# Optimization experiments

Hardware: AMD Instinct MI355X
Metric: run time of the kernel (lower is better)

The kernel has to match this reference:

```python
import jax, jax.numpy as jnp
import numpy as np

N_MELS, HIDDEN, HEAD_DIM = 80, 128, 64


def _gru_step(h, gx_t, w_hh, b_hh):
    # PyTorch GRU cell math. gx_t = x_t @ W_ih^T + b_ih, precomputed. [B, 3H]
    H = h.shape[-1]
    gh = h @ w_hh.T + b_hh  # [B, 3H]
    r = jax.nn.sigmoid(gx_t[:, :H] + gh[:, :H])
    z = jax.nn.sigmoid(gx_t[:, H:2 * H] + gh[:, H:2 * H])
    n = jnp.tanh(gx_t[:, 2 * H:] + r * gh[:, 2 * H:])
    return (1.0 - z) * n + z * h


def setup_inputs() -> dict:
    key = jax.random.key(0)
    ks = jax.random.split(key, 14)
    s = 1.0 / np.sqrt(HIDDEN)
    u = lambda k, shape, sc: jax.random.uniform(k, shape, jnp.float32, -sc, sc)
    return {
        "x": jax.random.normal(ks[0], (128, 1500, N_MELS), dtype=jnp.float32),
        # forward-direction GRU params
        "w_ih_f": u(ks[1], (3 * HIDDEN, N_MELS), s),
        "w_hh_f": u(ks[2], (3 * HIDDEN, HIDDEN), s),
        "b_ih_f": u(ks[3], (3 * HIDDEN,), s),
        "b_hh_f": u(ks[4], (3 * HIDDEN,), s),
        # backward-direction GRU params
        "w_ih_b": u(ks[5], (3 * HIDDEN, N_MELS), s),
        "w_hh_b": u(ks[6], (3 * HIDDEN, HIDDEN), s),
        "b_ih_b": u(ks[7], (3 * HIDDEN,), s),
        "b_hh_b": u(ks[8], (3 * HIDDEN,), s),
        # MLP head: Linear(2H, 64) -> ReLU -> Linear(64, 1)
        "w1": u(ks[9], (HEAD_DIM, 2 * HIDDEN), 1.0 / np.sqrt(2 * HIDDEN)),
        "b1": u(ks[10], (HEAD_DIM,), 1.0 / np.sqrt(2 * HIDDEN)),
        "w2": u(ks[11], (1, HEAD_DIM), 1.0 / np.sqrt(HEAD_DIM)),
        "b2": u(ks[12], (1,), 1.0 / np.sqrt(HEAD_DIM)),
    }


def reference(x, w_ih_f, w_hh_f, b_ih_f, b_hh_f, w_ih_b, w_hh_b, b_ih_b, b_hh_b, w1, b1, w2, b2):
    B, T, _ = x.shape
    h0 = jnp.zeros((B, HIDDEN), dtype=x.dtype)

    # Forward direction: last output = final hidden state after full scan.
    # Precompute input projections for all timesteps in one GEMM.
    gx_f = jnp.einsum('bti,gi->tbg', x, w_ih_f) + b_ih_f  # [T, B, 3H]
    h_f, _ = jax.lax.scan(lambda h, g: (_gru_step(h, g, w_hh_f, b_hh_f), None), h0, gx_f)

    # Backward direction: out[:, -1, H:] in PyTorch is the backward hidden
    # after processing ONLY x[:, -1] (the reverse scan's first step), so a
    # single GRU step from h0 reproduces it exactly.
    gx_b_last = x[:, -1, :] @ w_ih_b.T + b_ih_b  # [B, 3H]
    h_b = _gru_step(h0, gx_b_last, w_hh_b, b_hh_b)

    last = jnp.concatenate([h_f, h_b], axis=-1)  # [B, 2H]
    # Head (eval mode: dropout is identity)
    hdn = jax.nn.relu(last @ w1.T + b1)
    out = hdn @ w2.T + b2  # [B, 1]
    return out[:, 0]
```

## Files before the change

kernel.cpp:

```cpp
#include <hip/hip_runtime.h>

#define B 128
#define T 1500
#define NI 80
#define H 128
#define G 384
#define GT 64
#define NTT 128

typedef float v2f __attribute__((ext_vector_type(2)));

__device__ __forceinline__ float sigf(float x) { return 1.0f / (1.0f + __expf(-x)); }
__device__ __forceinline__ float tanhfast(float x) { return 1.0f - 2.0f / (1.0f + __expf(2.0f * x)); }
__device__ __forceinline__ v2f pkfma(v2f a, v2f b, v2f c) { return __builtin_elementwise_fma(a, b, c); }

__device__ __forceinline__ float sum8(float v) {
    int a = __builtin_bit_cast(int, v);
    float m = __builtin_bit_cast(float, __builtin_amdgcn_update_dpp(0, a, 0x141, 0xF, 0xF, true));
    float s = v + m;
    a = __builtin_bit_cast(int, s);
    m = __builtin_bit_cast(float, __builtin_amdgcn_update_dpp(0, a, 0x1B, 0xF, 0xF, true));
    s = s + m;
    a = __builtin_bit_cast(int, s);
    m = __builtin_bit_cast(float, __builtin_amdgcn_update_dpp(0, a, 0xB1, 0xF, 0xF, true));
    return s + m;
}

__global__ __launch_bounds__(256, 2)
void gx_gemm_kernel(const float* __restrict__ x, const float* __restrict__ w_ih,
                    const float* __restrict__ b_ih, float* __restrict__ gxT,
                    int t0, int ct) {
    __shared__ __align__(16) float wT[80][GT + 2];
    __shared__ __align__(16) float xT[80][NTT + 4];
    __shared__ float bias_s[GT];
    int tid = threadIdx.x;
    int b = blockIdx.z;
    int g0b = blockIdx.y * GT;
    int tt0 = blockIdx.x * NTT;

    for (int i = tid; i < GT * 20; i += 256) {
        int g = i & (GT - 1);
        int kc = i >> 6;
        float4 v = *(const float4*)(w_ih + (size_t)(g0b + g) * NI + 4 * kc);
        wT[4 * kc + 0][g] = v.x; wT[4 * kc + 1][g] = v.y;
        wT[4 * kc + 2][g] = v.z; wT[4 * kc + 3][g] = v.w;
    }
    for (int i = tid; i < NTT * 20; i += 256) {
        int c = i & (NTT - 1);
        int kc = i >> 7;
        int tt = tt0 + c; if (tt > ct - 1) tt = ct - 1;
        float4 v = *(const float4*)(x + ((size_t)b * T + (size_t)(t0 + tt)) * NI + 4 * kc);
        xT[4 * kc + 0][c] = v.x; xT[4 * kc + 1][c] = v.y;
        xT[4 * kc + 2][c] = v.z; xT[4 * kc + 3][c] = v.w;
    }
    if (tid < GT) bias_s[tid] = b_ih[g0b + tid];
    __syncthreads();

    int gi = tid & 15;
    int ti = tid >> 4;
    v2f acc[4][4];
#pragma unroll
    for (int r = 0; r < 4; ++r)
#pragma unroll
        for (int j = 0; j < 4; ++j) acc[r][j] = v2f{0.f, 0.f};

#pragma unroll 2
    for (int k = 0; k < 80; ++k) {
        const v2f* wv = (const v2f*)&wT[k][4 * gi];
        v2f w01 = wv[0], w23 = wv[1];
        const float4* xv = (const float4*)&xT[k][8 * ti];
        float4 x03 = xv[0], x47 = xv[1];
        v2f xp0 = {x03.x, x03.y}, xp1 = {x03.z, x03.w};
        v2f xp2 = {x47.x, x47.y}, xp3 = {x47.z, x47.w};
        float wr[4] = {w01.x, w01.y, w23.x, w23.y};
#pragma unroll
        for (int r = 0; r < 4; ++r) {
            v2f ws = {wr[r], wr[r]};
            acc[r][0] = pkfma(ws, xp0, acc[r][0]);
            acc[r][1] = pkfma(ws, xp1, acc[r][1]);
            acc[r][2] = pkfma(ws, xp2, acc[r][2]);
            acc[r][3] = pkfma(ws, xp3, acc[r][3]);
        }
    }
    __syncthreads();

    float (*ot)[NTT + 4] = (float (*)[NTT + 4])xT;
#pragma unroll
    for (int r = 0; r < 4; ++r) {
        float bias = bias_s[4 * gi + r];
#pragma unroll
        for (int j = 0; j < 4; ++j) {
            float2 o; o.x = acc[r][j].x + bias; o.y = acc[r][j].y + bias;
            *(float2*)&ot[4 * gi + r][8 * ti + 2 * j] = o;
        }
    }
    __syncthreads();

    for (int i = tid; i < GT * (NTT / 4); i += 256) {
        int row = i >> 5;
        int col = i & 31;
        int t = tt0 + 4 * col;
        if (t < ct) {
            float4 v = *(const float4*)&ot[row][4 * col];
            *(float4*)(gxT + ((size_t)b * G + g0b + row) * ct + t) = v;
        }
    }
}

__global__ __launch_bounds__(512)
__attribute__((amdgpu_waves_per_eu(2, 2)))
void scan_kernel(const float* __restrict__ gxT, const float* __restrict__ w_hh,
                 const float* __restrict__ b_hh, float* __restrict__ h_state,
                 int ct, int first, int last,
                 const float* __restrict__ x,
                 const float* __restrict__ w_ih_b, const float* __restrict__ b_ih_b,
                 const float* __restrict__ b_hh_b,
                 const float* __restrict__ w1, const float* __restrict__ b1,
                 const float* __restrict__ w2, const float* __restrict__ b2,
                 float* __restrict__ out) {
    int b = blockIdx.x;
    int tid = threadIdx.x;
    int jp = tid >> 3;
    int q = tid & 7;
    int j0 = jp, j1 = jp + 64;
    int jsel = (q < 4) ? j0 : j1;
    int hsel = ((jsel >> 4) * 20) + (jsel & 15);
    bool writer = (q & 3) == 0;

    __shared__ __align__(16) float hs[2][160];
    __shared__ __align__(16) float tail_gx[G];
    __shared__ __align__(16) float last_s[2 * H];
    __shared__ __align__(16) float xb_s[NI];

    v2f W0r[8], W0z[8], W0n[8], W1r[8], W1z[8], W1n[8];
    {
        const float* wb = w_hh + 16 * q;
        const v2f* p0 = (const v2f*)(wb + (size_t)j0 * H);
        const v2f* p1 = (const v2f*)(wb + (size_t)(j0 + H) * H);
        const v2f* p2 = (const v2f*)(wb + (size_t)(j0 + 2 * H) * H);
        const v2f* p3 = (const v2f*)(wb + (size_t)j1 * H);
        const v2f* p4 = (const v2f*)(wb + (size_t)(j1 + H) * H);
        const v2f* p5 = (const v2f*)(wb + (size_t)(j1 + 2 * H) * H);
#pragma unroll
        for (int i = 0; i < 8; ++i) {
            W0r[i] = p0[i]; W0z[i] = p1[i]; W0n[i] = p2[i];
            W1r[i] = p3[i]; W1z[i] = p4[i]; W1n[i] = p5[i];
        }
    }
#pragma unroll
    for (int i = 0; i < 8; ++i) {
        asm volatile("" : "+v"(W0r[i]), "+v"(W0z[i]), "+v"(W0n[i]),
                          "+v"(W1r[i]), "+v"(W1z[i]), "+v"(W1n[i]));
    }
    float br = b_hh[jsel], bz = b_hh[jsel + H], bn = b_hh[jsel + 2 * H];

    float h_cur = 0.f;
    if (!first) h_cur = h_state[b * H + jsel];
    if (writer) hs[0][hsel] = h_cur;

    const float* gp0 = gxT + ((size_t)b * G + jsel) * ct;
    const float* gp1 = gp0 + (size_t)H * ct;
    const float* gp2 = gp0 + (size_t)(2 * H) * ct;

    float4 A0, A1, A2, B0, B1, B2;
    A0 = *(const float4*)(gp0); A1 = *(const float4*)(gp1); A2 = *(const float4*)(gp2);
    {
        int t4 = (ct - 4 < 4) ? (ct - 4) : 4;
        B0 = *(const float4*)(gp0 + t4); B1 = *(const float4*)(gp1 + t4); B2 = *(const float4*)(gp2 + t4);
    }
    __syncthreads();

    auto dostep = [&](float g0, float g1, float g2, const float* SRC, float* DST) {
        const float4* hv4 = (const float4*)(SRC + 20 * q);
        float4 h0 = hv4[0], h1 = hv4[1], h2 = hv4[2], h3 = hv4[3];
        v2f a0r = {0.f, 0.f}, a0z = {0.f, 0.f}, a0n = {0.f, 0.f};
        v2f a1r = {0.f, 0.f}, a1z = {0.f, 0.f}, a1n = {0.f, 0.f};
        float4 hh[4] = {h0, h1, h2, h3};
#pragma unroll
        for (int i = 0; i < 4; ++i) {
            v2f hl = {hh[i].x, hh[i].y}, hg = {hh[i].z, hh[i].w};
            a0r = pkfma(W0r[2 * i], hl, a0r); a0r = pkfma(W0r[2 * i + 1], hg, a0r);
            a0z = pkfma(W0z[2 * i], hl, a0z); a0z = pkfma(W0z[2 * i + 1], hg, a0z);
            a0n = pkfma(W0n[2 * i], hl, a0n); a0n = pkfma(W0n[2 * i + 1], hg, a0n);
            a1r = pkfma(W1r[2 * i], hl, a1r); a1r = pkfma(W1r[2 * i + 1], hg, a1r);
            a1z = pkfma(W1z[2 * i], hl, a1z); a1z = pkfma(W1z[2 * i + 1], hg, a1z);
            a1n = pkfma(W1n[2 * i], hl, a1n); a1n = pkfma(W1n[2 * i + 1], hg, a1n);
        }
        float s0r = sum8(a0r.x + a0r.y), s0z = sum8(a0z.x + a0z.y), s0n = sum8(a0n.x + a0n.y);
        float s1r = sum8(a1r.x + a1r.y), s1z = sum8(a1z.x + a1z.y), s1n = sum8(a1n.x + a1n.y);
        bool lo = q < 4;
        float ar = lo ? s0r : s1r;
        float az = lo ? s0z : s1z;
        float an = lo ? s0n : s1n;
        float r = sigf(g0 + br + ar);
        float z = sigf(g1 + bz + az);
        float n = tanhfast(g2 + r * (bn + an));
        h_cur = n + z * (h_cur - n);
        if (writer) DST[hsel] = h_cur;
        asm volatile("s_waitcnt lgkmcnt(0)\n\ts_barrier" ::: "memory");
    };

    auto superstep = [&](int TL, float4& S0, float4& S1, float4& S2) {
        float l00 = S0.x, l01 = S0.y, l02 = S0.z, l03 = S0.w;
        float l10 = S1.x, l11 = S1.y, l12 = S1.z, l13 = S1.w;
        float l20 = S2.x, l21 = S2.y, l22 = S2.z, l23 = S2.w;
        int tpf = TL + 8; if (tpf > ct - 4) tpf = ct - 4;
        S0 = *(const float4*)(gp0 + tpf);
        S1 = *(const float4*)(gp1 + tpf);
        S2 = *(const float4*)(gp2 + tpf);
        dostep(l00, l10, l20, hs[0], hs[1]);
        dostep(l01, l11, l21, hs[1], hs[0]);
        dostep(l02, l12, l22, hs[0], hs[1]);
        dostep(l03, l13, l23, hs[1], hs[0]);
    };

    int tl = 0;
    for (; tl + 8 <= ct; tl += 8) {
        superstep(tl, A0, A1, A2);
        superstep(tl + 4, B0, B1, B2);
    }
    if (tl < ct) superstep(tl, A0, A1, A2);

    if (!last) {
        if (writer) h_state[b * H + jsel] = h_cur;
        return;
    }

    if (tid < NI) xb_s[tid] = x[((size_t)b * T + (T - 1)) * NI + tid];
    if (writer) last_s[jsel] = h_cur;
    __syncthreads();

    if (tid < G) {
        const float4* wbr = (const float4*)(w_ih_b + (size_t)tid * NI);
        const float4* xv = (const float4*)xb_s;
        float a0 = 0.f, a1 = 0.f, a2 = 0.f, a3 = 0.f;
#pragma unroll
        for (int i = 0; i < 20; ++i) {
            float4 wv = wbr[i]; float4 x4 = xv[i];
            a0 = fmaf(wv.x, x4.x, a0); a1 = fmaf(wv.y, x4.y, a1);
            a2 = fmaf(wv.z, x4.z, a2); a3 = fmaf(wv.w, x4.w, a3);
        }
        tail_gx[tid] = b_ih_b[tid] + ((a0 + a1) + (a2 + a3));
    }
    __syncthreads();

    if (tid < H) {
        float r = sigf(tail_gx[tid] + b_hh_b[tid]);
        float z = sigf(tail_gx[tid + H] + b_hh_b[tid + H]);
        float n = tanhfast(tail_gx[tid + 2 * H] + r * b_hh_b[tid + 2 * H]);
        last_s[H + tid] = (1.f - z) * n;
    }
    __syncthreads();

    if (tid < 64) {
        const float4* w1r = (const float4*)(w1 + (size_t)tid * 2 * H);
        const float4* lv = (const float4*)last_s;
        float a0 = 0.f, a1 = 0.f, a2 = 0.f, a3 = 0.f;
#pragma unroll
        for (int i = 0; i < 64; ++i) {
            float4 wv = w1r[i]; float4 l4 = lv[i];
            a0 = fmaf(wv.x, l4.x, a0); a1 = fmaf(wv.y, l4.y, a1);
            a2 = fmaf(wv.z, l4.z, a2); a3 = fmaf(wv.w, l4.w, a3);
        }
        float v = b1[tid] + ((a0 + a1) + (a2 + a3));
        v = fmaxf(v, 0.f) * w2[tid];
#pragma unroll
        for (int off = 32; off > 0; off >>= 1) v += __shfl_down(v, off);
        if (tid == 0) out[b] = v + b2[0];
    }
}

extern "C" void kernel_launch(void* const* d_in, const int* in_sizes, int n_in,
                              void* d_out, int out_size, void* d_ws, size_t ws_size,
                              hipStream_t stream) {
    (void)in_sizes; (void)n_in; (void)out_size;
    const float* x      = (const float*)d_in[0];
    const float* w_ih_f = (const float*)d_in[1];
    const float* w_hh_f = (const float*)d_in[2];
    const float* b_ih_f = (const float*)d_in[3];
    const float* b_hh_f = (const float*)d_in[4];
    const float* w_ih_b = (const float*)d_in[5];
    const float* w_hh_b = (const float*)d_in[6];
    const float* b_ih_b = (const float*)d_in[7];
    const float* b_hh_b = (const float*)d_in[8];
    const float* w1     = (const float*)d_in[9];
    const float* b1     = (const float*)d_in[10];
    const float* w2     = (const float*)d_in[11];
    const float* b2     = (const float*)d_in[12];
    (void)w_hh_b;
    float* out = (float*)d_out;

    float* h_state = (float*)d_ws;
    float* gxbuf = h_state + B * H;
    size_t hbytes = (size_t)B * H * sizeof(float);
    size_t avail = ws_size > hbytes ? ws_size - hbytes : 0;
    long long chunkT = (long long)(avail / ((size_t)B * G * sizeof(float)));
    chunkT &= ~3LL;
    if (chunkT > T) chunkT = T;
    if (chunkT < 4) chunkT = 4;

    for (int t0 = 0; t0 < T; t0 += (int)chunkT) {
        int ct = (T - t0 < (int)chunkT) ? (T - t0) : (int)chunkT;
        int ttiles = (ct + NTT - 1) / NTT;
        gx_gemm_kernel<<<dim3(ttiles, G / GT, B), dim3(256), 0, stream>>>(
            x, w_ih_f, b_ih_f, gxbuf, t0, ct);
        scan_kernel<<<dim3(B), dim3(512), 0, stream>>>(
            gxbuf, w_hh_f, b_hh_f, h_state, ct,
            (t0 == 0) ? 1 : 0, (t0 + ct >= T) ? 1 : 0,
            x, w_ih_b, b_ih_b, b_hh_b, w1, b1, w2, b2, out);
    }
}
```

Before: 1.118 ms.

## Fuse input-projection GEMM with recurrent scan and double-buffer chunks to overlap them

After: 962.8 us. 13.9% less time.

```diff
diff --git a/kernel.cpp b/kernel.cpp
--- a/kernel.cpp
+++ b/kernel.cpp
@@ -7,6 +7,10 @@
 #define G 384
 #define GT 64
 #define NTT 128
+
+#define WSZ (80 * (GT + 2))
+#define XSZ (80 * (NTT + 4))
+#define SMEM_FLOATS (WSZ + XSZ + GT)
 
 typedef float v2f __attribute__((ext_vector_type(2)));
 
@@ -26,247 +30,261 @@
     return s + m;
 }
 
-__global__ __launch_bounds__(256, 2)
-void gx_gemm_kernel(const float* __restrict__ x, const float* __restrict__ w_ih,
-                    const float* __restrict__ b_ih, float* __restrict__ gxT,
-                    int t0, int ct) {
-    __shared__ __align__(16) float wT[80][GT + 2];
-    __shared__ __align__(16) float xT[80][NTT + 4];
-    __shared__ float bias_s[GT];
-    int tid = threadIdx.x;
-    int b = blockIdx.z;
-    int g0b = blockIdx.y * GT;
-    int tt0 = blockIdx.x * NTT;
-
-    for (int i = tid; i < GT * 20; i += 256) {
-        int g = i & (GT - 1);
-        int kc = i >> 6;
-        float4 v = *(const float4*)(w_ih + (size_t)(g0b + g) * NI + 4 * kc);
-        wT[4 * kc + 0][g] = v.x; wT[4 * kc + 1][g] = v.y;
-        wT[4 * kc + 2][g] = v.z; wT[4 * kc + 3][g] = v.w;
-    }
-    for (int i = tid; i < NTT * 20; i += 256) {
-        int c = i & (NTT - 1);
-        int kc = i >> 7;
-        int tt = tt0 + c; if (tt > ct - 1) tt = ct - 1;
-        float4 v = *(const float4*)(x + ((size_t)b * T + (size_t)(t0 + tt)) * NI + 4 * kc);
-        xT[4 * kc + 0][c] = v.x; xT[4 * kc + 1][c] = v.y;
-        xT[4 * kc + 2][c] = v.z; xT[4 * kc + 3][c] = v.w;
-    }
-    if (tid < GT) bias_s[tid] = b_ih[g0b + tid];
-    __syncthreads();
-
-    int gi = tid & 15;
-    int ti = tid >> 4;
-    v2f acc[4][4];
-#pragma unroll
-    for (int r = 0; r < 4; ++r)
-#pragma unroll
-        for (int j = 0; j < 4; ++j) acc[r][j] = v2f{0.f, 0.f};
-
-#pragma unroll 2
-    for (int k = 0; k < 80; ++k) {
-        const v2f* wv = (const v2f*)&wT[k][4 * gi];
-        v2f w01 = wv[0], w23 = wv[1];
-        const float4* xv = (const float4*)&xT[k][8 * ti];
-        float4 x03 = xv[0], x47 = xv[1];
-        v2f xp0 = {x03.x, x03.y}, xp1 = {x03.z, x03.w};
-        v2f xp2 = {x47.x, x47.y}, xp3 = {x47.z, x47.w};
-        float wr[4] = {w01.x, w01.y, w23.x, w23.y};
-#pragma unroll
-        for (int r = 0; r < 4; ++r) {
-            v2f ws = {wr[r], wr[r]};
-            acc[r][0] = pkfma(ws, xp0, acc[r][0]);
-            acc[r][1] = pkfma(ws, xp1, acc[r][1]);
-            acc[r][2] = pkfma(ws, xp2, acc[r][2]);
-            acc[r][3] = pkfma(ws, xp3, acc[r][3]);
-        }
-    }
-    __syncthreads();
-
-    float (*ot)[NTT + 4] = (float (*)[NTT + 4])xT;
-#pragma unroll
-    for (int r = 0; r < 4; ++r) {
-        float bias = bias_s[4 * gi + r];
-#pragma unroll
-        for (int j = 0; j < 4; ++j) {
-            float2 o; o.x = acc[r][j].x + bias; o.y = acc[r][j].y + bias;
-            *(float2*)&ot[4 * gi + r][8 * ti + 2 * j] = o;
-        }
-    }
-    __syncthreads();
-
-    for (int i = tid; i < GT * (NTT / 4); i += 256) {
-        int row = i >> 5;
-        int col = i & 31;
-        int t = tt0 + 4 * col;
-        if (t < ct) {
-            float4 v = *(const float4*)&ot[row][4 * col];
-            *(float4*)(gxT + ((size_t)b * G + g0b + row) * ct + t) = v;
-        }
-    }
-}
-
 __global__ __launch_bounds__(512)
 __attribute__((amdgpu_waves_per_eu(2, 2)))
-void scan_kernel(const float* __restrict__ gxT, const float* __restrict__ w_hh,
-                 const float* __restrict__ b_hh, float* __restrict__ h_state,
-                 int ct, int first, int last,
-                 const float* __restrict__ x,
-                 const float* __restrict__ w_ih_b, const float* __restrict__ b_ih_b,
-                 const float* __restrict__ b_hh_b,
-                 const float* __restrict__ w1, const float* __restrict__ b1,
-                 const float* __restrict__ w2, const float* __restrict__ b2,
-                 float* __restrict__ out) {
-    int b = blockIdx.x;
+void fused_kernel(const float* __restrict__ x,
+                  const float* __restrict__ w_ih, const float* __restrict__ b_ih,
+                  const float* __restrict__ gx_read, int ct_read, int first, int last,
+                  float* __restrict__ gx_write, int t0_write, int ct_write,
+                  const float* __restrict__ w_hh, const float* __restrict__ b_hh,
+                  float* __restrict__ h_state,
+                  const float* __restrict__ w_ih_b, const float* __restrict__ b_ih_b,
+                  const float* __restrict__ b_hh_b,
+                  const float* __restrict__ w1, const float* __restrict__ b1,
+                  const float* __restrict__ w2, const float* __restrict__ b2,
+                  float* __restrict__ out) {
+    __shared__ __align__(16) float smem[SMEM_FLOATS];
     int tid = threadIdx.x;
-    int jp = tid >> 3;
-    int q = tid & 7;
-    int j0 = jp, j1 = jp + 64;
-    int jsel = (q < 4) ? j0 : j1;
-    int hsel = ((jsel >> 4) * 20) + (jsel & 15);
-    bool writer = (q & 3) == 0;
-
-    __shared__ __align__(16) float hs[2][160];
-    __shared__ __align__(16) float tail_gx[G];
-    __shared__ __align__(16) float last_s[2 * H];
-    __shared__ __align__(16) float xb_s[NI];
-
-    v2f W0r[8], W0z[8], W0n[8], W1r[8], W1z[8], W1n[8];
-    {
-        const float* wb = w_hh + 16 * q;
-        const v2f* p0 = (const v2f*)(wb + (size_t)j0 * H);
-        const v2f* p1 = (const v2f*)(wb + (size_t)(j0 + H) * H);
-        const v2f* p2 = (const v2f*)(wb + (size_t)(j0 + 2 * H) * H);
-        const v2f* p3 = (const v2f*)(wb + (size_t)j1 * H);
-        const v2f* p4 = (const v2f*)(wb + (size_t)(j1 + H) * H);
-        const v2f* p5 = (const v2f*)(wb + (size_t)(j1 + 2 * H) * H);
+    int scanBlocks = (ct_read > 0) ? B : 0;
+
+    if ((int)blockIdx.x < scanBlocks) {
+        const float* gxT = gx_read;
+        int ct = ct_read;
+        int b = blockIdx.x;
+        int jp = tid >> 3;
+        int q = tid & 7;
+        int j0 = jp, j1 = jp + 64;
+        int jsel = (q < 4) ? j0 : j1;
+        int hsel = ((jsel >> 4) * 20) + (jsel & 15);
+        bool writer = (q & 3) == 0;
+
+        float* hsA     = smem;
+        float* hsB     = smem + 160;
+        float* tail_gx = smem + 320;
+        float* last_s  = smem + 704;
+        float* xb_s    = smem + 960;
+
+        v2f W0r[8], W0z[8], W0n[8], W1r[8], W1z[8], W1n[8];
+        {
+            const float* wb = w_hh + 16 * q;
+            const v2f* p0 = (const v2f*)(wb + (size_t)j0 * H);
+            const v2f* p1 = (const v2f*)(wb + (size_t)(j0 + H) * H);
+            const v2f* p2 = (const v2f*)(wb + (size_t)(j0 + 2 * H) * H);
+            const v2f* p3 = (const v2f*)(wb + (size_t)j1 * H);
+            const v2f* p4 = (const v2f*)(wb + (size_t)(j1 + H) * H);
+            const v2f* p5 = (const v2f*)(wb + (size_t)(j1 + 2 * H) * H);
+#pragma unroll
+            for (int i = 0; i < 8; ++i) {
+                W0r[i] = p0[i]; W0z[i] = p1[i]; W0n[i] = p2[i];
+                W1r[i] = p3[i]; W1z[i] = p4[i]; W1n[i] = p5[i];
+            }
+        }
 #pragma unroll
         for (int i = 0; i < 8; ++i) {
-            W0r[i] = p0[i]; W0z[i] = p1[i]; W0n[i] = p2[i];
-            W1r[i] = p3[i]; W1z[i] = p4[i]; W1n[i] = p5[i];
-        }
-    }
-#pragma unroll
-    for (int i = 0; i < 8; ++i) {
-        asm volatile("" : "+v"(W0r[i]), "+v"(W0z[i]), "+v"(W0n[i]),
-                          "+v"(W1r[i]), "+v"(W1z[i]), "+v"(W1n[i]));
-    }
-    float br = b_hh[jsel], bz = b_hh[jsel + H], bn = b_hh[jsel + 2 * H];
-
-    float h_cur = 0.f;
-    if (!first) h_cur = h_state[b * H + jsel];
-    if (writer) hs[0][hsel] = h_cur;
-
-    const float* gp0 = gxT + ((size_t)b * G + jsel) * ct;
-    const float* gp1 = gp0 + (size_t)H * ct;
-    const float* gp2 = gp0 + (size_t)(2 * H) * ct;
-
-    float4 A0, A1, A2, B0, B1, B2;
-    A0 = *(const float4*)(gp0); A1 = *(const float4*)(gp1); A2 = *(const float4*)(gp2);
-    {
-        int t4 = (ct - 4 < 4) ? (ct - 4) : 4;
-        B0 = *(const float4*)(gp0 + t4); B1 = *(const float4*)(gp1 + t4); B2 = *(const float4*)(gp2 + t4);
-    }
-    __syncthreads();
-
-    auto dostep = [&](float g0, float g1, float g2, const float* SRC, float* DST) {
-        const float4* hv4 = (const float4*)(SRC + 20 * q);
-        float4 h0 = hv4[0], h1 = hv4[1], h2 = hv4[2], h3 = hv4[3];
-        v2f a0r = {0.f, 0.f}, a0z = {0.f, 0.f}, a0n = {0.f, 0.f};
-        v2f a1r = {0.f, 0.f}, a1z = {0.f, 0.f}, a1n = {0.f, 0.f};
-        float4 hh[4] = {h0, h1, h2, h3};
-#pragma unroll
-        for (int i = 0; i < 4; ++i) {
-            v2f hl = {hh[i].x, hh[i].y}, hg = {hh[i].z, hh[i].w};
-            a0r = pkfma(W0r[2 * i], hl, a0r); a0r = pkfma(W0r[2 * i + 1], hg, a0r);
-            a0z = pkfma(W0z[2 * i], hl, a0z); a0z = pkfma(W0z[2 * i + 1], hg, a0z);
-            a0n = pkfma(W0n[2 * i], hl, a0n); a0n = pkfma(W0n[2 * i + 1], hg, a0n);
-            a1r = pkfma(W1r[2 * i], hl, a1r); a1r = pkfma(W1r[2 * i + 1], hg, a1r);
-            a1z = pkfma(W1z[2 * i], hl, a1z); a1z = pkfma(W1z[2 * i + 1], hg, a1z);
-            a1n = pkfma(W1n[2 * i], hl, a1n); a1n = pkfma(W1n[2 * i + 1], hg, a1n);
-        }
-        float s0r = sum8(a0r.x + a0r.y), s0z = sum8(a0z.x + a0z.y), s0n = sum8(a0n.x + a0n.y);
-        float s1r = sum8(a1r.x + a1r.y), s1z = sum8(a1z.x + a1z.y), s1n = sum8(a1n.x + a1n.y);
-        bool lo = q < 4;
-        float ar = lo ? s0r : s1r;
-        float az = lo ? s0z : s1z;
-        float an = lo ? s0n : s1n;
-        float r = sigf(g0 + br + ar);
-        float z = sigf(g1 + bz + az);
-        float n = tanhfast(g2 + r * (bn + an));
-        h_cur = n + z * (h_cur - n);
-        if (writer) DST[hsel] = h_cur;
-        asm volatile("s_waitcnt lgkmcnt(0)\n\ts_barrier" ::: "memory");
-    };
-
-    auto superstep = [&](int TL, float4& S0, float4& S1, float4& S2) {
-        float l00 = S0.x, l01 = S0.y, l02 = S0.z, l03 = S0.w;
-        float l10 = S1.x, l11 = S1.y, l12 = S1.z, l13 = S1.w;
-        float l20 = S2.x, l21 = S2.y, l22 = S2.z, l23 = S2.w;
-        int tpf = TL + 8; if (tpf > ct - 4) tpf = ct - 4;
-        S0 = *(const float4*)(gp0 + tpf);
-        S1 = *(const float4*)(gp1 + tpf);
-        S2 = *(const float4*)(gp2 + tpf);
-        dostep(l00, l10, l20, hs[0], hs[1]);
-        dostep(l01, l11, l21, hs[1], hs[0]);
-        dostep(l02, l12, l22, hs[0], hs[1]);
-        dostep(l03, l13, l23, hs[1], hs[0]);
-    };
-
-    int tl = 0;
-    for (; tl + 8 <= ct; tl += 8) {
-        superstep(tl, A0, A1, A2);
-        superstep(tl + 4, B0, B1, B2);
-    }
-    if (tl < ct) superstep(tl, A0, A1, A2);
-
-    if (!last) {
-        if (writer) h_state[b * H + jsel] = h_cur;
+            asm volatile("" : "+v"(W0r[i]), "+v"(W0z[i]), "+v"(W0n[i]),
+                              "+v"(W1r[i]), "+v"(W1z[i]), "+v"(W1n[i]));
+        }
+        float br = b_hh[jsel], bz = b_hh[jsel + H], bn = b_hh[jsel + 2 * H];
+
+        float h_cur = 0.f;
+        if (!first) h_cur = h_state[b * H + jsel];
+        if (writer) hsA[hsel] = h_cur;
+
+        const float* gp0 = gxT + ((size_t)b * G + jsel) * ct;
+        const float* gp1 = gp0 + (size_t)H * ct;
+        const float* gp2 = gp0 + (size_t)(2 * H) * ct;
+
+        float4 A0, A1, A2, B0, B1, B2;
+        A0 = *(const float4*)(gp0); A1 = *(const float4*)(gp1); A2 = *(const float4*)(gp2);
+        {
+            int t4 = (ct - 4 < 4) ? (ct - 4) : 4;
+            B0 = *(const float4*)(gp0 + t4); B1 = *(const float4*)(gp1 + t4); B2 = *(const float4*)(gp2 + t4);
+        }
+        __syncthreads();
+
+        auto dostep = [&](float g0, float g1, float g2, const float* SRC, float* DST) {
+            const float4* hv4 = (const float4*)(SRC + 20 * q);
+            float4 h0 = hv4[0], h1 = hv4[1], h2 = hv4[2], h3 = hv4[3];
+            v2f a0r = {0.f, 0.f}, a0z = {0.f, 0.f}, a0n = {0.f, 0.f};
+            v2f a1r = {0.f, 0.f}, a1z = {0.f, 0.f}, a1n = {0.f, 0.f};
+            float4 hh[4] = {h0, h1, h2, h3};
+#pragma unroll
+            for (int i = 0; i < 4; ++i) {
+                v2f hl = {hh[i].x, hh[i].y}, hg = {hh[i].z, hh[i].w};
+                a0r = pkfma(W0r[2 * i], hl, a0r); a0r = pkfma(W0r[2 * i + 1], hg, a0r);
+                a0z = pkfma(W0z[2 * i], hl, a0z); a0z = pkfma(W0z[2 * i + 1], hg, a0z);
+                a0n = pkfma(W0n[2 * i], hl, a0n); a0n = pkfma(W0n[2 * i + 1], hg, a0n);
+                a1r = pkfma(W1r[2 * i], hl, a1r); a1r = pkfma(W1r[2 * i + 1], hg, a1r);
+                a1z = pkfma(W1z[2 * i], hl, a1z); a1z = pkfma(W1z[2 * i + 1], hg, a1z);
+                a1n = pkfma(W1n[2 * i], hl, a1n); a1n = pkfma(W1n[2 * i + 1], hg, a1n);
+            }
+            float s0r = sum8(a0r.x + a0r.y), s0z = sum8(a0z.x + a0z.y), s0n = sum8(a0n.x + a0n.y);
+            float s1r = sum8(a1r.x + a1r.y), s1z = sum8(a1z.x + a1z.y), s1n = sum8(a1n.x + a1n.y);
+            bool lo = q < 4;
+            float ar = lo ? s0r : s1r;
+            float az = lo ? s0z : s1z;
+            float an = lo ? s0n : s1n;
+            float r = sigf(g0 + br + ar);
+            float z = sigf(g1 + bz + az);
+            float n = tanhfast(g2 + r * (bn + an));
+            h_cur = n + z * (h_cur - n);
+            if (writer) DST[hsel] = h_cur;
+            asm volatile("s_waitcnt lgkmcnt(0)\n\ts_barrier" ::: "memory");
+        };
+
+        auto superstep = [&](int TL, float4& S0, float4& S1, float4& S2) {
+            float l00 = S0.x, l01 = S0.y, l02 = S0.z, l03 = S0.w;
+            float l10 = S1.x, l11 = S1.y, l12 = S1.z, l13 = S1.w;
+            float l20 = S2.x, l21 = S2.y, l22 = S2.z, l23 = S2.w;
+            int tpf = TL + 8; if (tpf > ct - 4) tpf = ct - 4;
+            S0 = *(const float4*)(gp0 + tpf);
+            S1 = *(const float4*)(gp1 + tpf);
+            S2 = *(const float4*)(gp2 + tpf);
+            dostep(l00, l10, l20, hsA, hsB);
+            dostep(l01, l11, l21, hsB, hsA);
+            dostep(l02, l12, l22, hsA, hsB);
+            dostep(l03, l13, l23, hsB, hsA);
+        };
+
+        int tl = 0;
+        for (; tl + 8 <= ct; tl += 8) {
+            superstep(tl, A0, A1, A2);
+            superstep(tl + 4, B0, B1, B2);
+        }
+        if (tl < ct) superstep(tl, A0, A1, A2);
+
+        if (!last) {
+            if (writer) h_state[b * H + jsel] = h_cur;
+            return;
+        }
+
+        if (tid < NI) xb_s[tid] = x[((size_t)b * T + (T - 1)) * NI + tid];
+        if (writer) last_s[jsel] = h_cur;
+        __syncthreads();
+
+        if (tid < G) {
+            const float4* wbr = (const float4*)(w_ih_b + (size_t)tid * NI);
+            const float4* xv = (const float4*)xb_s;
+            float a0 = 0.f, a1 = 0.f, a2 = 0.f, a3 = 0.f;
+#pragma unroll
+            for (int i = 0; i < 20; ++i) {
+                float4 wv = wbr[i]; float4 x4 = xv[i];
+                a0 = fmaf(wv.x, x4.x, a0); a1 = fmaf(wv.y, x4.y, a1);
+                a2 = fmaf(wv.z, x4.z, a2); a3 = fmaf(wv.w, x4.w, a3);
+            }
+            tail_gx[tid] = b_ih_b[tid] + ((a0 + a1) + (a2 + a3));
+        }
+        __syncthreads();
+
+        if (tid < H) {
+            float r = sigf(tail_gx[tid] + b_hh_b[tid]);
+            float z = sigf(tail_gx[tid + H] + b_hh_b[tid + H]);
+            float n = tanhfast(tail_gx[tid + 2 * H] + r * b_hh_b[tid + 2 * H]);
+            last_s[H + tid] = (1.f - z) * n;
+        }
+        __syncthreads();
+
+        if (tid < 64) {
+            const float4* w1r = (const float4*)(w1 + (size_t)tid * 2 * H);
+            const float4* lv = (const float4*)last_s;
+            float a0 = 0.f, a1 = 0.f, a2 = 0.f, a3 = 0.f;
+#pragma unroll
+            for (int i = 0; i < 64; ++i) {
+                float4 wv = w1r[i]; float4 l4 = lv[i];
+                a0 = fmaf(wv.x, l4.x, a0); a1 = fmaf(wv.y, l4.y, a1);
+                a2 = fmaf(wv.z, l4.z, a2); a3 = fmaf(wv.w, l4.w, a3);
+            }
+            float v = b1[tid] + ((a0 + a1) + (a2 + a3));
+            v = fmaxf(v, 0.f) * w2[tid];
+#pragma unroll
+            for (int off = 32; off > 0; off >>= 1) v += __shfl_down(v, off);
+            if (tid == 0) out[b] = v + b2[0];
+        }
         return;
     }
 
-    if (tid < NI) xb_s[tid] = x[((size_t)b * T + (T - 1)) * NI + tid];
-    if (writer) last_s[jsel] = h_cur;
-    __syncthreads();
-
-    if (tid < G) {
-        const float4* wbr = (const float4*)(w_ih_b + (size_t)tid * NI);
-        const float4* xv = (const float4*)xb_s;
-        float a0 = 0.f, a1 = 0.f, a2 = 0.f, a3 = 0.f;
-#pragma unroll
-        for (int i = 0; i < 20; ++i) {
-            float4 wv = wbr[i]; float4 x4 = xv[i];
-            a0 = fmaf(wv.x, x4.x, a0); a1 = fmaf(wv.y, x4.y, a1);
-            a2 = fmaf(wv.z, x4.z, a2); a3 = fmaf(wv.w, x4.w, a3);
-        }
-        tail_gx[tid] = b_ih_b[tid] + ((a0 + a1) + (a2 + a3));
-    }
-    __syncthreads();
-
-    if (tid < H) {
-        float r = sigf(tail_gx[tid] + b_hh_b[tid]);
-        float z = sigf(tail_gx[tid + H] + b_hh_b[tid + H]);
-        float n = tanhfast(tail_gx[tid + 2 * H] + r * b_hh_b[tid + 2 * H]);
-        last_s[H + tid] = (1.f - z) * n;
-    }
-    __syncthreads();
-
-    if (tid < 64) {
-        const float4* w1r = (const float4*)(w1 + (size_t)tid * 2 * H);
-        const float4* lv = (const float4*)last_s;
-        float a0 = 0.f, a1 = 0.f, a2 = 0.f, a3 = 0.f;
-#pragma unroll
-        for (int i = 0; i < 64; ++i) {
-            float4 wv = w1r[i]; float4 l4 = lv[i];
-            a0 = fmaf(wv.x, l4.x, a0); a1 = fmaf(wv.y, l4.y, a1);
-            a2 = fmaf(wv.z, l4.z, a2); a3 = fmaf(wv.w, l4.w, a3);
-        }
-        float v = b1[tid] + ((a0 + a1) + (a2 + a3));
-        v = fmaxf(v, 0.f) * w2[tid];
-#pragma unroll
-        for (int off = 32; off > 0; off >>= 1) v += __shfl_down(v, off);
-        if (tid == 0) out[b] = v + b2[0];
+    if (ct_write <= 0) return;
+    {
+        float* wT = smem;
+        float* xT = smem + WSZ;
+        float* bias_s = smem + WSZ + XSZ;
+        int ct = ct_write;
+        int t0 = t0_write;
+        int gb = blockIdx.x - scanBlocks;
+        int ngb = gridDim.x - scanBlocks;
+        int ttiles = (ct + NTT - 1) / NTT;
+        int jobs = ttiles * (G / GT) * B;
+        int gi = tid & 15;
+        int ti = tid >> 4;
+
+        for (int job = gb; job < jobs; job += ngb) {
+            int tile = job % ttiles;
+            int rem = job / ttiles;
+            int gy = rem % (G / GT);
+            int b = rem / (G / GT);
+            int g0b = gy * GT;
+            int tt0 = tile * NTT;
+
+            __syncthreads();
+            for (int i = tid; i < GT * 20; i += 512) {
+                int g = i & (GT - 1);
+                int kc = i >> 6;
+                float4 v = *(const float4*)(w_ih + (size_t)(g0b + g) * NI + 4 * kc);
+                wT[(4 * kc + 0) * (GT + 2) + g] = v.x; wT[(4 * kc + 1) * (GT + 2) + g] = v.y;
+                wT[(4 * kc + 2) * (GT + 2) + g] = v.z; wT[(4 * kc + 3) * (GT + 2) + g] = v.w;
+            }
+            for (int i = tid; i < NTT * 20; i += 512) {
+                int c = i & (NTT - 1);
+                int kc = i >> 7;
+                int tt = tt0 + c; if (tt > ct - 1) tt = ct - 1;
+                float4 v = *(const float4*)(x + ((size_t)b * T + (size_t)(t0 + tt)) * NI + 4 * kc);
+                xT[(4 * kc + 0) * (NTT + 4) + c] = v.x; xT[(4 * kc + 1) * (NTT + 4) + c] = v.y;
+                xT[(4 * kc + 2) * (NTT + 4) + c] = v.z; xT[(4 * kc + 3) * (NTT + 4) + c] = v.w;
+            }
+            if (tid < GT) bias_s[tid] = b_ih[g0b + tid];
+            __syncthreads();
+
+            v2f acc[4][2];
+#pragma unroll
+            for (int r = 0; r < 4; ++r) { acc[r][0] = v2f{0.f, 0.f}; acc[r][1] = v2f{0.f, 0.f}; }
+
+#pragma unroll 2
+            for (int k = 0; k < 80; ++k) {
+                const v2f* wv = (const v2f*)&wT[k * (GT + 2) + 4 * gi];
+                v2f w01 = wv[0], w23 = wv[1];
+                float4 x03 = *(const float4*)&xT[k * (NTT + 4) + 4 * ti];
+                v2f xp0 = {x03.x, x03.y}, xp1 = {x03.z, x03.w};
+                float wr[4] = {w01.x, w01.y, w23.x, w23.y};
+#pragma unroll
+                for (int r = 0; r < 4; ++r) {
+                    v2f ws = {wr[r], wr[r]};
+                    acc[r][0] = pkfma(ws, xp0, acc[r][0]);
+                    acc[r][1] = pkfma(ws, xp1, acc[r][1]);
+                }
+            }
+            __syncthreads();
+
+#pragma unroll
+            for (int r = 0; r < 4; ++r) {
+                float bias = bias_s[4 * gi + r];
+                float2 o0, o1;
+                o0.x = acc[r][0].x + bias; o0.y = acc[r][0].y + bias;
+                o1.x = acc[r][1].x + bias; o1.y = acc[r][1].y + bias;
+                *(float2*)&xT[(4 * gi + r) * (NTT + 4) + 4 * ti]     = o0;
+                *(float2*)&xT[(4 * gi + r) * (NTT + 4) + 4 * ti + 2] = o1;
+            }
+            __syncthreads();
+
+            for (int i = tid; i < GT * (NTT / 4); i += 512) {
+                int row = i >> 5;
+                int col = i & 31;
+                int t = tt0 + 4 * col;
+                if (t < ct) {
+                    float4 v = *(const float4*)&xT[row * (NTT + 4) + 4 * col];
+                    *(float4*)(gx_write + ((size_t)b * G + g0b + row) * ct + t) = v;
+                }
+            }
+        }
     }
 }
 
@@ -291,22 +309,40 @@
     float* out = (float*)d_out;
 
     float* h_state = (float*)d_ws;
-    float* gxbuf = h_state + B * H;
+    float* buf0 = h_state + B * H;
     size_t hbytes = (size_t)B * H * sizeof(float);
     size_t avail = ws_size > hbytes ? ws_size - hbytes : 0;
-    long long chunkT = (long long)(avail / ((size_t)B * G * sizeof(float)));
-    chunkT &= ~3LL;
-    if (chunkT > T) chunkT = T;
-    if (chunkT < 4) chunkT = 4;
-
-    for (int t0 = 0; t0 < T; t0 += (int)chunkT) {
-        int ct = (T - t0 < (int)chunkT) ? (T - t0) : (int)chunkT;
-        int ttiles = (ct + NTT - 1) / NTT;
-        gx_gemm_kernel<<<dim3(ttiles, G / GT, B), dim3(256), 0, stream>>>(
-            x, w_ih_f, b_ih_f, gxbuf, t0, ct);
-        scan_kernel<<<dim3(B), dim3(512), 0, stream>>>(
-            gxbuf, w_hh_f, b_hh_f, h_state, ct,
-            (t0 == 0) ? 1 : 0, (t0 + ct >= T) ? 1 : 0,
-            x, w_ih_b, b_ih_b, b_hh_b, w1, b1, w2, b2, out);
+
+    long long chunk = 376;
+    size_t per = (size_t)B * G * sizeof(float);
+    if (avail < 2 * per * (size_t)chunk) {
+        long long c = (long long)(avail / (2 * per)) & ~3LL;
+        chunk = c;
+    }
+    if (chunk > T) chunk = T;
+    if (chunk < 4) chunk = 4;
+
+    float* bufs[2] = { buf0, buf0 + (size_t)B * G * (size_t)chunk };
+
+    int cs0 = (T < (int)chunk) ? T : (int)chunk;
+    fused_kernel<<<dim3(256), dim3(512), 0, stream>>>(
+        x, w_ih_f, b_ih_f,
+        nullptr, 0, 0, 0,
+        bufs[0], 0, cs0,
+        w_hh_f, b_hh_f, h_state,
+        w_ih_b, b_ih_b, b_hh_b, w1, b1, w2, b2, out);
+
+    int i = 0;
+    for (int t0 = 0; t0 < T; ++i) {
+        int cs = (T - t0 < (int)chunk) ? (T - t0) : (int)chunk;
+        int nt0 = t0 + cs;
+        int csn = (nt0 < T) ? ((T - nt0 < (int)chunk) ? (T - nt0) : (int)chunk) : 0;
+        fused_kernel<<<dim3(256), dim3(512), 0, stream>>>(
+            x, w_ih_f, b_ih_f,
+            bufs[i & 1], cs, (t0 == 0) ? 1 : 0, (nt0 >= T) ? 1 : 0,
+            bufs[(i + 1) & 1], nt0, csn,
+            w_hh_f, b_hh_f, h_state,
+            w_ih_b, b_ih_b, b_hh_b, w1, b1, w2, b2, out);
+        t0 = nt0;
     }
 }
```
